# Optimization experiments

Hardware: AMD Instinct MI355X
Metric: run time of the kernel (lower is better)

Reference implementation:

```python
import jax, jax.numpy as jnp
import numpy as np

IMG_W, IMG_H = 960.0, 512.0
HM_W, HM_H = 240, 128
GRID_SIZE = (8000.0, 8000.0, 2000.0)
CUBE = (80, 80, 20)


def setup_inputs() -> dict:
    rng = np.random.default_rng(0)
    B, N, J = 8, 5, 15
    heatmaps = jnp.asarray(rng.random((B, N, J, HM_H, HM_W)).astype(np.float32))
    center3d = np.array([0.0, -500.0, 800.0])
    grid_center = jnp.asarray(np.tile(center3d.astype(np.float32), (B, 1)))
    Rs, Ts = [], []
    for v in range(N):  # cameras on a ring looking at the space center
        ang = 2.0 * np.pi * v / N
        cam_pos = center3d + np.array([5000.0 * np.cos(ang), 5000.0 * np.sin(ang), 1200.0])
        z = center3d - cam_pos; z = z / np.linalg.norm(z)
        x = np.cross(z, np.array([0.0, 0.0, 1.0])); x = x / np.linalg.norm(x)
        y = np.cross(z, x)
        Rs.append(np.stack([x, y, z])); Ts.append(cam_pos)
    R = jnp.asarray(np.tile(np.stack(Rs)[None], (B, 1, 1, 1)).astype(np.float32))
    T = jnp.asarray(np.tile(np.stack(Ts)[None], (B, 1, 1)).astype(np.float32))
    f = jnp.full((B, N, 2), 1500.0, jnp.float32)
    c = jnp.asarray(np.tile(np.array([IMG_W / 2, IMG_H / 2], np.float32), (B, N, 1)))
    k = jnp.asarray((1e-4 * rng.standard_normal((B, N, 3))).astype(np.float32))
    p = jnp.asarray((1e-4 * rng.standard_normal((B, N, 2))).astype(np.float32))
    cam_center = jnp.asarray(np.tile(np.array([IMG_W / 2, IMG_H / 2], np.float32), (B, N, 1)))
    scale = jnp.asarray(np.tile(np.array([IMG_W / 200.0, IMG_H / 200.0], np.float32), (B, N, 1)))
    return dict(heatmaps=heatmaps, grid_center=grid_center, R=R, T=T, f=f, c=c,
                k=k, p=p, cam_center=cam_center, scale=scale)


def _compute_grid(center):  # center [3] -> [nbins,3], meshgrid 'ij' like torch
    ax = [jnp.linspace(-GRID_SIZE[d] / 2, GRID_SIZE[d] / 2, CUBE[d]) + center[d] for d in range(3)]
    X, Y, Z = jnp.meshgrid(*ax, indexing='ij')
    return jnp.stack([X.ravel(), Y.ravel(), Z.ravel()], axis=1)


def _bilinear(img, x, y):  # img [J,H,W], x,y [N]; zero padding, align_corners=True
    x0 = jnp.floor(x); y0 = jnp.floor(y)
    dx = x - x0; dy = y - y0
    def tap(ix, iy, w):
        valid = (ix >= 0) & (ix < HM_W) & (iy >= 0) & (iy < HM_H)
        ii = jnp.clip(ix, 0, HM_W - 1).astype(jnp.int32)
        jj = jnp.clip(iy, 0, HM_H - 1).astype(jnp.int32)
        return img[:, jj, ii] * (w * valid)[None, :]
    return (tap(x0, y0, (1 - dx) * (1 - dy)) + tap(x0 + 1, y0, dx * (1 - dy)) +
            tap(x0, y0 + 1, (1 - dx) * dy) + tap(x0 + 1, y0 + 1, dx * dy))


def _per_cam(hm, grid, R, T, f, c, k, p, cc, sc):
    # pinhole projection with radial/tangential distortion (voxelpose project_pose)
    xcam = R @ (grid - T).T                       # [3,N]
    yn = xcam[:2] / (xcam[2] + 1e-5)              # [2,N]
    r2 = yn[0] ** 2 + yn[1] ** 2
    radial = 1.0 + k[0] * r2 + k[1] * r2 ** 2 + k[2] * r2 ** 3
    tan = p[0] * yn[1] + p[1] * yn[0]
    yd = yn * (radial + 2.0 * tan) + jnp.stack([p[1], p[0]])[:, None] * r2
    xy = (f[:, None] * yd + c[:, None]).T         # [N,2] pixel coords
    width = 2.0 * cc[0]; height = 2.0 * cc[1]
    mask = (xy[:, 0] >= 0) & (xy[:, 1] >= 0) & (xy[:, 0] < width) & (xy[:, 1] < height)
    xy = jnp.clip(xy, -1.0, jnp.maximum(width, height))
    # get_transform with rot=0: h = 200*scale[0]
    h200 = 200.0 * sc[0]
    res = jnp.array([IMG_W, IMG_H], jnp.float32)
    xy = xy * (res / h200) + res * (-cc / h200 + 0.5)
    xy = xy * jnp.array([HM_W, HM_H], jnp.float32) / res
    g = xy / jnp.array([HM_W - 1, HM_H - 1], jnp.float32) * 2.0 - 1.0
    g = jnp.clip(g, -1.1, 1.1)
    px = (g[:, 0] + 1.0) * 0.5 * (HM_W - 1)
    py = (g[:, 1] + 1.0) * 0.5 * (HM_H - 1)
    return _bilinear(hm, px, py), mask.astype(hm.dtype)  # [J,N], [N]


def _forward(heatmaps, grid_center, R, T, f, c, k, p, cam_center, scale):
    B, N, J = heatmaps.shape[:3]
    grids = jax.vmap(_compute_grid)(grid_center)  # [B,nbins,3]
    per_b = jax.vmap(_per_cam, in_axes=(0, None, 0, 0, 0, 0, 0, 0, 0, 0))
    vals, mask = jax.vmap(per_b)(heatmaps, grids, R, T, f, c, k, p, cam_center, scale)
    # vals [B,n,J,nbins], mask [B,n,nbins]: masked mean over cameras
    num = jnp.einsum('bnjv,bnv->bjv', vals, mask)
    den = jnp.sum(mask, axis=1) + 1e-6            # [B,nbins]
    cubes = num / den[:, None, :]
    cubes = jnp.nan_to_num(cubes)
    cubes = jnp.clip(cubes, 0.0, 1.0).reshape(B, J, *CUBE)
    return cubes, grids


def reference(heatmaps, grid_center, R, T, f, c, k, p, cam_center, scale):
    return _forward(heatmaps, grid_center, R, T, f, c, k, p, cam_center, scale)
```

## Files before the change

kernel.cpp:

```cpp
#include <hip/hip_runtime.h>

#define HM_W 240
#define HM_H 128
#define NCAM 5
#define NJ   15
#define CX   80
#define CY   80
#define CZ   20
#define NBINS (CX*CY*CZ)
#define NB   8
#define HWPIX (HM_H*HM_W)

__device__ __forceinline__ int iclamp(int x, int lo, int hi) {
    return x < lo ? lo : (x > hi ? hi : x);
}

#define PACK_CHUNKS ((NCAM * HWPIX) / 256)
__global__ void __launch_bounds__(256)
pack_u8(const float* __restrict__ hm, uint4* __restrict__ out)
{
    const int b = blockIdx.x & 7;
    const int chunk = blockIdx.x >> 3;
    const int pix = chunk * 256 + threadIdx.x;
    const int n = pix / HWPIX;
    const int yx = pix - n * HWPIX;
    const int bn = b * NCAM + n;
    const float* src = hm + (size_t)bn * NJ * HWPIX + yx;
    unsigned v8[16];
    #pragma unroll
    for (int j = 0; j < NJ; ++j) {
        float v = src[(size_t)j * HWPIX];
        v = fminf(fmaxf(v, 0.0f), 1.0f);
        v8[j] = (unsigned)fmaf(v, 255.0f, 0.5f);
    }
    v8[15] = 0u;
    uint4 q;
    q.x = v8[0]  | (v8[1]  << 8) | (v8[2]  << 16) | (v8[3]  << 24);
    q.y = v8[4]  | (v8[5]  << 8) | (v8[6]  << 16) | (v8[7]  << 24);
    q.z = v8[8]  | (v8[9]  << 8) | (v8[10] << 16) | (v8[11] << 24);
    q.w = v8[12] | (v8[13] << 8) | (v8[14] << 16);
    out[(size_t)bn * HWPIX + yx] = q;
}

struct TapsW {
    int i00, i10, i01, i11;
    unsigned W;
    float m;
};

__device__ __forceinline__ TapsW make_taps(
    float xc, float yc, float zc,
    float k0, float k1, float k2, float p0, float p1,
    float fx, float fy, float cxx, float cyy,
    float width, float height, float himax,
    float Ax, float Bx, float Ay, float By)
{
    const float inv = 1.0f / (zc + 1e-5f);
    const float yn0 = xc * inv;
    const float yn1 = yc * inv;
    const float r2 = yn0 * yn0 + yn1 * yn1;
    const float radial = 1.0f + k0 * r2 + k1 * (r2 * r2) + k2 * (r2 * r2 * r2);
    const float tan2 = 2.0f * (p0 * yn1 + p1 * yn0);
    const float yd0 = yn0 * (radial + tan2) + p1 * r2;
    const float yd1 = yn1 * (radial + tan2) + p0 * r2;

    float x = fmaf(fx, yd0, cxx);
    float y = fmaf(fy, yd1, cyy);

    const float m = (x >= 0.0f && y >= 0.0f && x < width && y < height) ? 1.0f : 0.0f;

    x = fminf(fmaxf(x, -1.0f), himax);
    y = fminf(fmaxf(y, -1.0f), himax);

    float gx = fmaf(Ax, x, Bx);
    float gy = fmaf(Ay, y, By);
    gx = fminf(fmaxf(gx, -1.1f), 1.1f);
    gy = fminf(fmaxf(gy, -1.1f), 1.1f);
    const float px = (gx + 1.0f) * (0.5f * (HM_W - 1));
    const float py = (gy + 1.0f) * (0.5f * (HM_H - 1));

    const float x0f = floorf(px), y0f = floorf(py);
    const float dx = px - x0f, dy = py - y0f;
    const int x0 = (int)x0f, y0 = (int)y0f;
    const int x1 = x0 + 1, y1 = y0 + 1;

    float w00 = (1.0f - dx) * (1.0f - dy);
    float w10 = dx * (1.0f - dy);
    float w01 = (1.0f - dx) * dy;
    float w11 = dx * dy;

    const bool vx0 = (x0 >= 0) & (x0 < HM_W);
    const bool vx1 = (x1 >= 0) & (x1 < HM_W);
    const bool vy0 = (y0 >= 0) & (y0 < HM_H);
    const bool vy1 = (y1 >= 0) & (y1 < HM_H);

    w00 = (vx0 && vy0) ? w00 * m : 0.0f;
    w10 = (vx1 && vy0) ? w10 * m : 0.0f;
    w01 = (vx0 && vy1) ? w01 * m : 0.0f;
    w11 = (vx1 && vy1) ? w11 * m : 0.0f;

    const unsigned wq0 = (unsigned)fmaf(w00, 255.0f, 0.5f);
    const unsigned wq1 = (unsigned)fmaf(w10, 255.0f, 0.5f);
    const unsigned wq2 = (unsigned)fmaf(w01, 255.0f, 0.5f);
    const unsigned wq3 = (unsigned)fmaf(w11, 255.0f, 0.5f);

    TapsW t;
    t.W = wq0 | (wq1 << 8) | (wq2 << 16) | (wq3 << 24);
    t.m = m;

    const int xa = iclamp(x0, 0, HM_W - 1);
    const int xb = iclamp(x1, 0, HM_W - 1);
    const int ya = iclamp(y0, 0, HM_H - 1);
    const int yb = iclamp(y1, 0, HM_H - 1);

    t.i00 = ya * HM_W + xa;
    t.i10 = ya * HM_W + xb;
    t.i01 = yb * HM_W + xa;
    t.i11 = yb * HM_W + xb;
    return t;
}

struct CamLoad {
    uint4 a00, a10, a01, a11;
    uint4 b00, b10, b01, b11;
    unsigned W0, W1;
    float m0, m1;
};

__device__ __forceinline__ CamLoad issue_cam(
    const uint4* __restrict__ hmp, int bn,
    float gx, float gy, float gz0, float gz1,
    const float* __restrict__ R, const float* __restrict__ T,
    const float* __restrict__ f, const float* __restrict__ c,
    const float* __restrict__ k, const float* __restrict__ p,
    const float* __restrict__ cc, const float* __restrict__ sc)
{
    const float* Rn = R + (size_t)bn * 9;
    const float* Tn = T + (size_t)bn * 3;

    const float X = gx - Tn[0];
    const float Y = gy - Tn[1];
    const float Z0 = gz0 - Tn[2];
    const float Z1 = gz1 - Tn[2];

    const float xp = Rn[0] * X + Rn[1] * Y;
    const float yp = Rn[3] * X + Rn[4] * Y;
    const float zp = Rn[6] * X + Rn[7] * Y;

    const float k0 = k[bn * 3 + 0], k1 = k[bn * 3 + 1], k2 = k[bn * 3 + 2];
    const float p0 = p[bn * 2 + 0], p1 = p[bn * 2 + 1];
    const float fx = f[bn * 2 + 0], fy = f[bn * 2 + 1];
    const float cxx = c[bn * 2 + 0], cyy = c[bn * 2 + 1];
    const float ccx = cc[bn * 2 + 0], ccy = cc[bn * 2 + 1];
    const float width = 2.0f * ccx, height = 2.0f * ccy;
    const float himax = fmaxf(width, height);

    const float inv_h = 1.0f / (200.0f * sc[bn * 2 + 0]);
    const float Ax = (2.0f * (float)HM_W / (float)(HM_W - 1)) * inv_h;
    const float Bx = (0.5f - ccx * inv_h) * (2.0f * (float)HM_W / (float)(HM_W - 1)) - 1.0f;
    const float Ay = (2.0f * (float)HM_H / (float)(HM_H - 1)) * inv_h;
    const float By = (0.5f - ccy * inv_h) * (2.0f * (float)HM_H / (float)(HM_H - 1)) - 1.0f;

    const TapsW t0 = make_taps(fmaf(Rn[2], Z0, xp), fmaf(Rn[5], Z0, yp), fmaf(Rn[8], Z0, zp),
                               k0, k1, k2, p0, p1, fx, fy, cxx, cyy,
                               width, height, himax, Ax, Bx, Ay, By);
    const TapsW t1 = make_taps(fmaf(Rn[2], Z1, xp), fmaf(Rn[5], Z1, yp), fmaf(Rn[8], Z1, zp),
                               k0, k1, k2, p0, p1, fx, fy, cxx, cyy,
                               width, height, himax, Ax, Bx, Ay, By);

    const uint4* base = hmp + (size_t)bn * HWPIX;
    CamLoad L;
    L.a00 = base[t0.i00]; L.a10 = base[t0.i10];
    L.a01 = base[t0.i01]; L.a11 = base[t0.i11];
    L.b00 = base[t1.i00]; L.b10 = base[t1.i10];
    L.b01 = base[t1.i01]; L.b11 = base[t1.i11];
    L.W0 = t0.W; L.W1 = t1.W;
    L.m0 = t0.m; L.m1 = t1.m;
    return L;
}

__device__ __forceinline__ void dot_taps(uint4 q00, uint4 q10, uint4 q01, uint4 q11,
                                         unsigned W, unsigned* __restrict__ acc)
{
    const unsigned* a00 = (const unsigned*)&q00;
    const unsigned* a10 = (const unsigned*)&q10;
    const unsigned* a01 = (const unsigned*)&q01;
    const unsigned* a11 = (const unsigned*)&q11;
    #pragma unroll
    for (int d = 0; d < 4; ++d) {
        const int jb = 4 * d;
        const unsigned pA = __builtin_amdgcn_perm(a00[d], a10[d], 0x01050004u);
        const unsigned pB = __builtin_amdgcn_perm(a01[d], a11[d], 0x01050004u);
        acc[jb + 0] = __builtin_amdgcn_udot4(
            __builtin_amdgcn_perm(pA, pB, 0x01000504u), W, acc[jb + 0], false);
        acc[jb + 1] = __builtin_amdgcn_udot4(
            __builtin_amdgcn_perm(pA, pB, 0x03020706u), W, acc[jb + 1], false);
        const unsigned pC = __builtin_amdgcn_perm(a00[d], a10[d], 0x03070206u);
        const unsigned pD = __builtin_amdgcn_perm(a01[d], a11[d], 0x03070206u);
        acc[jb + 2] = __builtin_amdgcn_udot4(
            __builtin_amdgcn_perm(pC, pD, 0x01000504u), W, acc[jb + 2], false);
        if (jb + 3 < NJ)
            acc[jb + 3] = __builtin_amdgcn_udot4(
                __builtin_amdgcn_perm(pC, pD, 0x03020706u), W, acc[jb + 3], false);
    }
}

__device__ __forceinline__ void consume(const CamLoad& L,
                                        unsigned* __restrict__ acc0,
                                        unsigned* __restrict__ acc1,
                                        float& den0, float& den1)
{
    dot_taps(L.a00, L.a10, L.a01, L.a11, L.W0, acc0);
    dot_taps(L.b00, L.b10, L.b01, L.b11, L.W1, acc1);
    den0 += L.m0;
    den1 += L.m1;
}

#define PROJ_CHUNKS ((NBINS / 2) / 256)
__global__ void __launch_bounds__(256)
project_u8(const uint4* __restrict__ hmp,
           const float* __restrict__ grid_center,
           const float* __restrict__ R, const float* __restrict__ T,
           const float* __restrict__ f, const float* __restrict__ c,
           const float* __restrict__ k, const float* __restrict__ p,
           const float* __restrict__ cc, const float* __restrict__ sc,
           float* __restrict__ cubes, float* __restrict__ grids)
{
    const int b = blockIdx.x & 7;
    const int chunk = blockIdx.x >> 3;
    const int v2 = chunk * 256 + threadIdx.x;

    const int col = v2 / (CZ / 2);
    const int tz  = v2 - col * (CZ / 2);
    const int ix = col / CY;
    const int iy = col - ix * CY;
    const int iz0 = 2 * tz;
    const int v0 = col * CZ + iz0;

    const float gcx = grid_center[b * 3 + 0];
    const float gcy = grid_center[b * 3 + 1];
    const float gcz = grid_center[b * 3 + 2];

    const float gx = -4000.0f + (float)ix * (8000.0f / 79.0f) + gcx;
    const float gy = -4000.0f + (float)iy * (8000.0f / 79.0f) + gcy;
    const float gz0 = -1000.0f + (float)iz0 * (2000.0f / 19.0f) + gcz;
    const float gz1 = gz0 + (2000.0f / 19.0f);

    {
        float* g = grids + ((size_t)b * NBINS + v0) * 3;
        float2* g2 = reinterpret_cast<float2*>(g);
        g2[0] = make_float2(gx, gy);
        g2[1] = make_float2(gz0, gx);
        g2[2] = make_float2(gy, gz1);
    }

    unsigned acc0[NJ], acc1[NJ];
    #pragma unroll
    for (int j = 0; j < NJ; ++j) { acc0[j] = 0u; acc1[j] = 0u; }
    float den0 = 1e-6f, den1 = 1e-6f;

    const int bn0 = b * NCAM;

    CamLoad A = issue_cam(hmp, bn0 + 0, gx, gy, gz0, gz1, R, T, f, c, k, p, cc, sc);
    CamLoad Bv = issue_cam(hmp, bn0 + 1, gx, gy, gz0, gz1, R, T, f, c, k, p, cc, sc);

    consume(A, acc0, acc1, den0, den1);
    A = issue_cam(hmp, bn0 + 2, gx, gy, gz0, gz1, R, T, f, c, k, p, cc, sc);

    consume(Bv, acc0, acc1, den0, den1);
    Bv = issue_cam(hmp, bn0 + 3, gx, gy, gz0, gz1, R, T, f, c, k, p, cc, sc);

    consume(A, acc0, acc1, den0, den1);
    A = issue_cam(hmp, bn0 + 4, gx, gy, gz0, gz1, R, T, f, c, k, p, cc, sc);

    consume(Bv, acc0, acc1, den0, den1);
    consume(A, acc0, acc1, den0, den1);

    const float s0 = (1.0f / 65025.0f) / den0;
    const float s1 = (1.0f / 65025.0f) / den1;
    const size_t outbase = (size_t)b * NJ * NBINS + v0;
    #pragma unroll
    for (int j = 0; j < NJ; ++j) {
        float2 o;
        o.x = fminf((float)acc0[j] * s0, 1.0f);
        o.y = fminf((float)acc1[j] * s1, 1.0f);
        *reinterpret_cast<float2*>(cubes + outbase + (size_t)j * NBINS) = o;
    }
}

__global__ void __launch_bounds__(256)
project_direct(const float* __restrict__ hm,
               const float* __restrict__ grid_center,
               const float* __restrict__ R, const float* __restrict__ T,
               const float* __restrict__ f, const float* __restrict__ c,
               const float* __restrict__ k, const float* __restrict__ p,
               const float* __restrict__ cc, const float* __restrict__ sc,
               float* __restrict__ cubes, float* __restrict__ grids)
{
    const int b = blockIdx.y;
    const int v = blockIdx.x * blockDim.x + threadIdx.x;
    if (v >= NBINS) return;

    const int ix = v / (CY * CZ);
    const int rem = v - ix * (CY * CZ);
    const int iy = rem / CZ;
    const int iz = rem - iy * CZ;

    const float gx = -4000.0f + (float)ix * (8000.0f / 79.0f) + grid_center[b * 3 + 0];
    const float gy = -4000.0f + (float)iy * (8000.0f / 79.0f) + grid_center[b * 3 + 1];
    const float gz = -1000.0f + (float)iz * (2000.0f / 19.0f) + grid_center[b * 3 + 2];

    {
        float* g = grids + ((size_t)b * NBINS + v) * 3;
        g[0] = gx; g[1] = gy; g[2] = gz;
    }

    float num[NJ];
    #pragma unroll
    for (int j = 0; j < NJ; ++j) num[j] = 0.0f;
    float den = 1e-6f;

    for (int n = 0; n < NCAM; ++n) {
        const int bn = b * NCAM + n;
        const float* Rn = R + (size_t)bn * 9;
        const float* Tn = T + (size_t)bn * 3;
        const float X = gx - Tn[0], Y = gy - Tn[1], Z = gz - Tn[2];

        const float xc = Rn[0]*X + Rn[1]*Y + Rn[2]*Z;
        const float yc = Rn[3]*X + Rn[4]*Y + Rn[5]*Z;
        const float zc = Rn[6]*X + Rn[7]*Y + Rn[8]*Z;

        const float inv = 1.0f / (zc + 1e-5f);
        const float yn0 = xc * inv, yn1 = yc * inv;
        const float r2 = yn0*yn0 + yn1*yn1;
        const float k0 = k[bn*3+0], k1 = k[bn*3+1], k2 = k[bn*3+2];
        const float radial = 1.0f + k0*r2 + k1*r2*r2 + k2*r2*r2*r2;
        const float p0 = p[bn*2+0], p1 = p[bn*2+1];
        const float tan2 = 2.0f * (p0*yn1 + p1*yn0);
        const float yd0 = yn0*(radial+tan2) + p1*r2;
        const float yd1 = yn1*(radial+tan2) + p0*r2;

        float x = fmaf(f[bn*2+0], yd0, c[bn*2+0]);
        float y = fmaf(f[bn*2+1], yd1, c[bn*2+1]);

        const float ccx = cc[bn*2+0], ccy = cc[bn*2+1];
        const float width = 2.0f*ccx, height = 2.0f*ccy;
        const float m = (x >= 0.0f && y >= 0.0f && x < width && y < height) ? 1.0f : 0.0f;
        const float himax = fmaxf(width, height);
        x = fminf(fmaxf(x, -1.0f), himax);
        y = fminf(fmaxf(y, -1.0f), himax);

        const float inv_h = 1.0f / (200.0f * sc[bn*2+0]);
        float gxn = (x*inv_h + (0.5f - ccx*inv_h)) * (2.0f*(float)HM_W/(float)(HM_W-1)) - 1.0f;
        float gyn = (y*inv_h + (0.5f - ccy*inv_h)) * (2.0f*(float)HM_H/(float)(HM_H-1)) - 1.0f;
        gxn = fminf(fmaxf(gxn, -1.1f), 1.1f);
        gyn = fminf(fmaxf(gyn, -1.1f), 1.1f);
        const float px = (gxn + 1.0f) * (0.5f * (HM_W - 1));
        const float py = (gyn + 1.0f) * (0.5f * (HM_H - 1));

        const float x0f = floorf(px), y0f = floorf(py);
        const float dx = px - x0f, dy = py - y0f;
        const int x0 = (int)x0f, y0 = (int)y0f;
        const int x1 = x0 + 1, y1 = y0 + 1;

        float w00 = (1.0f-dx)*(1.0f-dy), w10 = dx*(1.0f-dy);
        float w01 = (1.0f-dx)*dy,        w11 = dx*dy;
        const bool vx0 = (x0 >= 0) & (x0 < HM_W);
        const bool vx1 = (x1 >= 0) & (x1 < HM_W);
        const bool vy0 = (y0 >= 0) & (y0 < HM_H);
        const bool vy1 = (y1 >= 0) & (y1 < HM_H);
        w00 = (vx0 && vy0) ? w00*m : 0.0f;
        w10 = (vx1 && vy0) ? w10*m : 0.0f;
        w01 = (vx0 && vy1) ? w01*m : 0.0f;
        w11 = (vx1 && vy1) ? w11*m : 0.0f;

        const int xa = iclamp(x0,0,HM_W-1), xb = iclamp(x1,0,HM_W-1);
        const int ya = iclamp(y0,0,HM_H-1), yb = iclamp(y1,0,HM_H-1);
        const int i00 = ya*HM_W+xa, i10 = ya*HM_W+xb, i01 = yb*HM_W+xa, i11 = yb*HM_W+xb;

        const float* base = hm + (size_t)bn * NJ * HWPIX;
        #pragma unroll
        for (int j = 0; j < NJ; ++j) {
            const float* img = base + (size_t)j * HWPIX;
            num[j] += w00*img[i00] + w10*img[i10] + w01*img[i01] + w11*img[i11];
        }
        den += m;
    }

    const float invden = 1.0f / den;
    const size_t outbase = (size_t)b * NJ * NBINS + v;
    #pragma unroll
    for (int j = 0; j < NJ; ++j) {
        float val = num[j] * invden;
        val = fminf(fmaxf(val, 0.0f), 1.0f);
        cubes[outbase + (size_t)j * NBINS] = val;
    }
}

extern "C" void kernel_launch(void* const* d_in, const int* in_sizes, int n_in,
                              void* d_out, int out_size, void* d_ws, size_t ws_size,
                              hipStream_t stream) {
    const float* hm = (const float*)d_in[0];
    const float* gc = (const float*)d_in[1];
    const float* R  = (const float*)d_in[2];
    const float* T  = (const float*)d_in[3];
    const float* f  = (const float*)d_in[4];
    const float* c  = (const float*)d_in[5];
    const float* k  = (const float*)d_in[6];
    const float* p  = (const float*)d_in[7];
    const float* cc = (const float*)d_in[8];
    const float* sc = (const float*)d_in[9];

    float* out   = (float*)d_out;
    float* cubes = out;
    float* grids = out + (size_t)NB * NJ * NBINS;

    const size_t need = (size_t)NB * NCAM * HWPIX * 16 + 64;
    if (ws_size >= need) {
        uint4* hmp = (uint4*)d_ws;
        hipLaunchKernelGGL(pack_u8, dim3(NB * PACK_CHUNKS), dim3(256), 0, stream,
                           hm, hmp);
        hipLaunchKernelGGL(project_u8, dim3(NB * PROJ_CHUNKS), dim3(256), 0, stream,
                           hmp, gc, R, T, f, c, k, p, cc, sc, cubes, grids);
    } else {
        dim3 grid((NBINS + 255) / 256, NB);
        hipLaunchKernelGGL(project_direct, grid, dim3(256), 0, stream,
                           hm, gc, R, T, f, c, k, p, cc, sc, cubes, grids);
    }
}
```

Measured before the change: 58.47 us.

## Pack vertically-paired heatmap texels so each bilinear column fetch is one 32-byte load

The pack kernel now writes each texel together with the texel one row below into a 32-byte pair. The projection kernel can then fetch both vertical taps of a bilinear sample as one contiguous 32-byte read per column, with a select for the top-row edge case. This halves the number of gather instructions, at the cost of doubling the packed workspace and its write traffic. Heatmap loads and output stores are also made nontemporal, the camera loop is simplified, and the older 16-byte path is kept as a fallback when the workspace is too small.

New measurement: 85.61 us. 1.46x slower.

```diff
diff --git a/kernel.cpp b/kernel.cpp
--- a/kernel.cpp
+++ b/kernel.cpp
@@ -1,4 +1,5 @@
 #include <hip/hip_runtime.h>
+#include <string.h>
 
 #define HM_W 240
 #define HM_H 128
@@ -15,21 +16,30 @@
     return x < lo ? lo : (x > hi ? hi : x);
 }
 
+__device__ __forceinline__ uint4 sel4(bool c, uint4 a, uint4 b) {
+    uint4 r;
+    r.x = c ? a.x : b.x;  r.y = c ? a.y : b.y;
+    r.z = c ? a.z : b.z;  r.w = c ? a.w : b.w;
+    return r;
+}
+
+
 #define PACK_CHUNKS ((NCAM * HWPIX) / 256)
 __global__ void __launch_bounds__(256)
-pack_u8(const float* __restrict__ hm, uint4* __restrict__ out)
+pack_vp(const float* __restrict__ hm, uint4* __restrict__ vp)
 {
     const int b = blockIdx.x & 7;
     const int chunk = blockIdx.x >> 3;
     const int pix = chunk * 256 + threadIdx.x;
     const int n = pix / HWPIX;
     const int yx = pix - n * HWPIX;
+    const int y = yx / HM_W;
     const int bn = b * NCAM + n;
     const float* src = hm + (size_t)bn * NJ * HWPIX + yx;
     unsigned v8[16];
     #pragma unroll
     for (int j = 0; j < NJ; ++j) {
-        float v = src[(size_t)j * HWPIX];
+        float v = __builtin_nontemporal_load(src + (size_t)j * HWPIX);
         v = fminf(fmaxf(v, 0.0f), 1.0f);
         v8[j] = (unsigned)fmaf(v, 255.0f, 0.5f);
     }
@@ -39,16 +49,21 @@
     q.y = v8[4]  | (v8[5]  << 8) | (v8[6]  << 16) | (v8[7]  << 24);
     q.z = v8[8]  | (v8[9]  << 8) | (v8[10] << 16) | (v8[11] << 24);
     q.w = v8[12] | (v8[13] << 8) | (v8[14] << 16);
-    out[(size_t)bn * HWPIX + yx] = q;
-}
-
-struct TapsW {
-    int i00, i10, i01, i11;
+
+    uint4* e = vp + ((size_t)bn * HWPIX + yx) * 2;
+    e[0] = q;
+    if (y > 0)      (e - 2 * HM_W)[1] = q;
+    if (y == HM_H - 1) e[1] = q;
+}
+
+struct TapsV {
+    int e0, e1;
     unsigned W;
     float m;
+    bool selB;
 };
 
-__device__ __forceinline__ TapsW make_taps(
+__device__ __forceinline__ TapsV make_tapsv(
     float xc, float yc, float zc,
     float k0, float k1, float k2, float p0, float p1,
     float fx, float fy, float cxx, float cyy,
@@ -104,79 +119,17 @@
     const unsigned wq2 = (unsigned)fmaf(w01, 255.0f, 0.5f);
     const unsigned wq3 = (unsigned)fmaf(w11, 255.0f, 0.5f);
 
-    TapsW t;
+    TapsV t;
     t.W = wq0 | (wq1 << 8) | (wq2 << 16) | (wq3 << 24);
     t.m = m;
+    t.selB = (y0 >= 0);
 
     const int xa = iclamp(x0, 0, HM_W - 1);
     const int xb = iclamp(x1, 0, HM_W - 1);
     const int ya = iclamp(y0, 0, HM_H - 1);
-    const int yb = iclamp(y1, 0, HM_H - 1);
-
-    t.i00 = ya * HM_W + xa;
-    t.i10 = ya * HM_W + xb;
-    t.i01 = yb * HM_W + xa;
-    t.i11 = yb * HM_W + xb;
+    t.e0 = ya * HM_W + xa;
+    t.e1 = ya * HM_W + xb;
     return t;
-}
-
-struct CamLoad {
-    uint4 a00, a10, a01, a11;
-    uint4 b00, b10, b01, b11;
-    unsigned W0, W1;
-    float m0, m1;
-};
-
-__device__ __forceinline__ CamLoad issue_cam(
-    const uint4* __restrict__ hmp, int bn,
-    float gx, float gy, float gz0, float gz1,
-    const float* __restrict__ R, const float* __restrict__ T,
-    const float* __restrict__ f, const float* __restrict__ c,
-    const float* __restrict__ k, const float* __restrict__ p,
-    const float* __restrict__ cc, const float* __restrict__ sc)
-{
-    const float* Rn = R + (size_t)bn * 9;
-    const float* Tn = T + (size_t)bn * 3;
-
-    const float X = gx - Tn[0];
-    const float Y = gy - Tn[1];
-    const float Z0 = gz0 - Tn[2];
-    const float Z1 = gz1 - Tn[2];
-
-    const float xp = Rn[0] * X + Rn[1] * Y;
-    const float yp = Rn[3] * X + Rn[4] * Y;
-    const float zp = Rn[6] * X + Rn[7] * Y;
-
-    const float k0 = k[bn * 3 + 0], k1 = k[bn * 3 + 1], k2 = k[bn * 3 + 2];
-    const float p0 = p[bn * 2 + 0], p1 = p[bn * 2 + 1];
-    const float fx = f[bn * 2 + 0], fy = f[bn * 2 + 1];
-    const float cxx = c[bn * 2 + 0], cyy = c[bn * 2 + 1];
-    const float ccx = cc[bn * 2 + 0], ccy = cc[bn * 2 + 1];
-    const float width = 2.0f * ccx, height = 2.0f * ccy;
-    const float himax = fmaxf(width, height);
-
-    const float inv_h = 1.0f / (200.0f * sc[bn * 2 + 0]);
-    const float Ax = (2.0f * (float)HM_W / (float)(HM_W - 1)) * inv_h;
-    const float Bx = (0.5f - ccx * inv_h) * (2.0f * (float)HM_W / (float)(HM_W - 1)) - 1.0f;
-    const float Ay = (2.0f * (float)HM_H / (float)(HM_H - 1)) * inv_h;
-    const float By = (0.5f - ccy * inv_h) * (2.0f * (float)HM_H / (float)(HM_H - 1)) - 1.0f;
-
-    const TapsW t0 = make_taps(fmaf(Rn[2], Z0, xp), fmaf(Rn[5], Z0, yp), fmaf(Rn[8], Z0, zp),
-                               k0, k1, k2, p0, p1, fx, fy, cxx, cyy,
-                               width, height, himax, Ax, Bx, Ay, By);
-    const TapsW t1 = make_taps(fmaf(Rn[2], Z1, xp), fmaf(Rn[5], Z1, yp), fmaf(Rn[8], Z1, zp),
-                               k0, k1, k2, p0, p1, fx, fy, cxx, cyy,
-                               width, height, himax, Ax, Bx, Ay, By);
-
-    const uint4* base = hmp + (size_t)bn * HWPIX;
-    CamLoad L;
-    L.a00 = base[t0.i00]; L.a10 = base[t0.i10];
-    L.a01 = base[t0.i01]; L.a11 = base[t0.i11];
-    L.b00 = base[t1.i00]; L.b10 = base[t1.i10];
-    L.b01 = base[t1.i01]; L.b11 = base[t1.i11];
-    L.W0 = t0.W; L.W1 = t1.W;
-    L.m0 = t0.m; L.m1 = t1.m;
-    return L;
 }
 
 __device__ __forceinline__ void dot_taps(uint4 q00, uint4 q10, uint4 q01, uint4 q11,
@@ -205,18 +158,216 @@
     }
 }
 
-__device__ __forceinline__ void consume(const CamLoad& L,
-                                        unsigned* __restrict__ acc0,
-                                        unsigned* __restrict__ acc1,
-                                        float& den0, float& den1)
-{
-    dot_taps(L.a00, L.a10, L.a01, L.a11, L.W0, acc0);
-    dot_taps(L.b00, L.b10, L.b01, L.b11, L.W1, acc1);
-    den0 += L.m0;
-    den1 += L.m1;
-}
-
 #define PROJ_CHUNKS ((NBINS / 2) / 256)
+__global__ void __launch_bounds__(256)
+project_vp(const uint4* __restrict__ vp,
+           const float* __restrict__ grid_center,
+           const float* __restrict__ R, const float* __restrict__ T,
+           const float* __restrict__ f, const float* __restrict__ c,
+           const float* __restrict__ k, const float* __restrict__ p,
+           const float* __restrict__ cc, const float* __restrict__ sc,
+           float* __restrict__ cubes, float* __restrict__ grids)
+{
+    const int b = blockIdx.x & 7;
+    const int chunk = blockIdx.x >> 3;
+    const int v2 = chunk * 256 + threadIdx.x;
+
+    const int col = v2 / (CZ / 2);
+    const int tz  = v2 - col * (CZ / 2);
+    const int ix = col / CY;
+    const int iy = col - ix * CY;
+    const int iz0 = 2 * tz;
+    const int v0 = col * CZ + iz0;
+
+    const float gcx = grid_center[b * 3 + 0];
+    const float gcy = grid_center[b * 3 + 1];
+    const float gcz = grid_center[b * 3 + 2];
+
+    const float gx = -4000.0f + (float)ix * (8000.0f / 79.0f) + gcx;
+    const float gy = -4000.0f + (float)iy * (8000.0f / 79.0f) + gcy;
+    const float gz0 = -1000.0f + (float)iz0 * (2000.0f / 19.0f) + gcz;
+    const float gz1 = gz0 + (2000.0f / 19.0f);
+
+    {
+        float* g = grids + ((size_t)b * NBINS + v0) * 3;
+        union { float2 f2; double d; } u0, u1, u2;
+        u0.f2 = make_float2(gx, gy);
+        u1.f2 = make_float2(gz0, gx);
+        u2.f2 = make_float2(gy, gz1);
+        __builtin_nontemporal_store(u0.d, (double*)(g + 0));
+        __builtin_nontemporal_store(u1.d, (double*)(g + 2));
+        __builtin_nontemporal_store(u2.d, (double*)(g + 4));
+    }
+
+    unsigned acc0[NJ], acc1[NJ];
+    #pragma unroll
+    for (int j = 0; j < NJ; ++j) { acc0[j] = 0u; acc1[j] = 0u; }
+    float den0 = 1e-6f, den1 = 1e-6f;
+
+    #pragma unroll
+    for (int n = 0; n < NCAM; ++n) {
+        const int bn = b * NCAM + n;
+        const float* Rn = R + (size_t)bn * 9;
+        const float* Tn = T + (size_t)bn * 3;
+
+        const float X = gx - Tn[0];
+        const float Y = gy - Tn[1];
+        const float Z0 = gz0 - Tn[2];
+        const float Z1 = gz1 - Tn[2];
+
+        const float xp = Rn[0] * X + Rn[1] * Y;
+        const float yp = Rn[3] * X + Rn[4] * Y;
+        const float zp = Rn[6] * X + Rn[7] * Y;
+
+        const float k0 = k[bn * 3 + 0], k1 = k[bn * 3 + 1], k2 = k[bn * 3 + 2];
+        const float p0 = p[bn * 2 + 0], p1 = p[bn * 2 + 1];
+        const float fx = f[bn * 2 + 0], fy = f[bn * 2 + 1];
+        const float cxx = c[bn * 2 + 0], cyy = c[bn * 2 + 1];
+        const float ccx = cc[bn * 2 + 0], ccy = cc[bn * 2 + 1];
+        const float width = 2.0f * ccx, height = 2.0f * ccy;
+        const float himax = fmaxf(width, height);
+
+        const float inv_h = 1.0f / (200.0f * sc[bn * 2 + 0]);
+        const float Ax = (2.0f * (float)HM_W / (float)(HM_W - 1)) * inv_h;
+        const float Bx = (0.5f - ccx * inv_h) * (2.0f * (float)HM_W / (float)(HM_W - 1)) - 1.0f;
+        const float Ay = (2.0f * (float)HM_H / (float)(HM_H - 1)) * inv_h;
+        const float By = (0.5f - ccy * inv_h) * (2.0f * (float)HM_H / (float)(HM_H - 1)) - 1.0f;
+
+        const TapsV t0 = make_tapsv(fmaf(Rn[2], Z0, xp), fmaf(Rn[5], Z0, yp), fmaf(Rn[8], Z0, zp),
+                                    k0, k1, k2, p0, p1, fx, fy, cxx, cyy,
+                                    width, height, himax, Ax, Bx, Ay, By);
+        const TapsV t1 = make_tapsv(fmaf(Rn[2], Z1, xp), fmaf(Rn[5], Z1, yp), fmaf(Rn[8], Z1, zp),
+                                    k0, k1, k2, p0, p1, fx, fy, cxx, cyy,
+                                    width, height, himax, Ax, Bx, Ay, By);
+
+        const uint4* base = vp + (size_t)bn * HWPIX * 2;
+
+        const uint4* e00 = base + 2 * t0.e0;
+        const uint4* e01 = base + 2 * t0.e1;
+        const uint4 a0lo = e00[0], a0hi = e00[1];
+        const uint4 a1lo = e01[0], a1hi = e01[1];
+        const uint4* e10 = base + 2 * t1.e0;
+        const uint4* e11 = base + 2 * t1.e1;
+        const uint4 b0lo = e10[0], b0hi = e10[1];
+        const uint4 b1lo = e11[0], b1hi = e11[1];
+
+        const uint4 qa0b = sel4(t0.selB, a0hi, a0lo);
+        const uint4 qa1b = sel4(t0.selB, a1hi, a1lo);
+        const uint4 qb0b = sel4(t1.selB, b0hi, b0lo);
+        const uint4 qb1b = sel4(t1.selB, b1hi, b1lo);
+
+        dot_taps(a0lo, a1lo, qa0b, qa1b, t0.W, acc0);
+        dot_taps(b0lo, b1lo, qb0b, qb1b, t1.W, acc1);
+        den0 += t0.m;
+        den1 += t1.m;
+    }
+
+    const float s0 = (1.0f / 65025.0f) / den0;
+    const float s1 = (1.0f / 65025.0f) / den1;
+    const size_t outbase = (size_t)b * NJ * NBINS + v0;
+    #pragma unroll
+    for (int j = 0; j < NJ; ++j) {
+        union { float2 f2; double d; } o;
+        o.f2.x = fminf((float)acc0[j] * s0, 1.0f);
+        o.f2.y = fminf((float)acc1[j] * s1, 1.0f);
+        __builtin_nontemporal_store(o.d, (double*)(cubes + outbase + (size_t)j * NBINS));
+    }
+}
+
+
+__global__ void __launch_bounds__(256)
+pack_u8(const float* __restrict__ hm, uint4* __restrict__ out)
+{
+    const int b = blockIdx.x & 7;
+    const int chunk = blockIdx.x >> 3;
+    const int pix = chunk * 256 + threadIdx.x;
+    const int n = pix / HWPIX;
+    const int yx = pix - n * HWPIX;
+    const int bn = b * NCAM + n;
+    const float* src = hm + (size_t)bn * NJ * HWPIX + yx;
+    unsigned v8[16];
+    #pragma unroll
+    for (int j = 0; j < NJ; ++j) {
+        float v = src[(size_t)j * HWPIX];
+        v = fminf(fmaxf(v, 0.0f), 1.0f);
+        v8[j] = (unsigned)fmaf(v, 255.0f, 0.5f);
+    }
+    v8[15] = 0u;
+    uint4 q;
+    q.x = v8[0]  | (v8[1]  << 8) | (v8[2]  << 16) | (v8[3]  << 24);
+    q.y = v8[4]  | (v8[5]  << 8) | (v8[6]  << 16) | (v8[7]  << 24);
+    q.z = v8[8]  | (v8[9]  << 8) | (v8[10] << 16) | (v8[11] << 24);
+    q.w = v8[12] | (v8[13] << 8) | (v8[14] << 16);
+    out[(size_t)bn * HWPIX + yx] = q;
+}
+
+struct TapsU {
+    int i00, i10, i01, i11;
+    unsigned W;
+    float m;
+};
+
+__device__ __forceinline__ TapsU make_taps16(
+    float xc, float yc, float zc,
+    float k0, float k1, float k2, float p0, float p1,
+    float fx, float fy, float cxx, float cyy,
+    float width, float height, float himax,
+    float Ax, float Bx, float Ay, float By)
+{
+    const float inv = 1.0f / (zc + 1e-5f);
+    const float yn0 = xc * inv;
+    const float yn1 = yc * inv;
+    const float r2 = yn0 * yn0 + yn1 * yn1;
+    const float radial = 1.0f + k0 * r2 + k1 * (r2 * r2) + k2 * (r2 * r2 * r2);
+    const float tan2 = 2.0f * (p0 * yn1 + p1 * yn0);
+    const float yd0 = yn0 * (radial + tan2) + p1 * r2;
+    const float yd1 = yn1 * (radial + tan2) + p0 * r2;
+
+    float x = fmaf(fx, yd0, cxx);
+    float y = fmaf(fy, yd1, cyy);
+    const float m = (x >= 0.0f && y >= 0.0f && x < width && y < height) ? 1.0f : 0.0f;
+    x = fminf(fmaxf(x, -1.0f), himax);
+    y = fminf(fmaxf(y, -1.0f), himax);
+    float gx = fmaf(Ax, x, Bx);
+    float gy = fmaf(Ay, y, By);
+    gx = fminf(fmaxf(gx, -1.1f), 1.1f);
+    gy = fminf(fmaxf(gy, -1.1f), 1.1f);
+    const float px = (gx + 1.0f) * (0.5f * (HM_W - 1));
+    const float py = (gy + 1.0f) * (0.5f * (HM_H - 1));
+    const float x0f = floorf(px), y0f = floorf(py);
+    const float dx = px - x0f, dy = py - y0f;
+    const int x0 = (int)x0f, y0 = (int)y0f;
+    const int x1 = x0 + 1, y1 = y0 + 1;
+    float w00 = (1.0f - dx) * (1.0f - dy);
+    float w10 = dx * (1.0f - dy);
+    float w01 = (1.0f - dx) * dy;
+    float w11 = dx * dy;
+    const bool vx0 = (x0 >= 0) & (x0 < HM_W);
+    const bool vx1 = (x1 >= 0) & (x1 < HM_W);
+    const bool vy0 = (y0 >= 0) & (y0 < HM_H);
+    const bool vy1 = (y1 >= 0) & (y1 < HM_H);
+    w00 = (vx0 && vy0) ? w00 * m : 0.0f;
+    w10 = (vx1 && vy0) ? w10 * m : 0.0f;
+    w01 = (vx0 && vy1) ? w01 * m : 0.0f;
+    w11 = (vx1 && vy1) ? w11 * m : 0.0f;
+    const unsigned wq0 = (unsigned)fmaf(w00, 255.0f, 0.5f);
+    const unsigned wq1 = (unsigned)fmaf(w10, 255.0f, 0.5f);
+    const unsigned wq2 = (unsigned)fmaf(w01, 255.0f, 0.5f);
+    const unsigned wq3 = (unsigned)fmaf(w11, 255.0f, 0.5f);
+    TapsU t;
+    t.W = wq0 | (wq1 << 8) | (wq2 << 16) | (wq3 << 24);
+    t.m = m;
+    const int xa = iclamp(x0, 0, HM_W - 1);
+    const int xb = iclamp(x1, 0, HM_W - 1);
+    const int ya = iclamp(y0, 0, HM_H - 1);
+    const int yb = iclamp(y1, 0, HM_H - 1);
+    t.i00 = ya * HM_W + xa;
+    t.i10 = ya * HM_W + xb;
+    t.i01 = yb * HM_W + xa;
+    t.i11 = yb * HM_W + xb;
+    return t;
+}
+
 __global__ void __launch_bounds__(256)
 project_u8(const uint4* __restrict__ hmp,
            const float* __restrict__ grid_center,
@@ -259,22 +410,43 @@
     for (int j = 0; j < NJ; ++j) { acc0[j] = 0u; acc1[j] = 0u; }
     float den0 = 1e-6f, den1 = 1e-6f;
 
-    const int bn0 = b * NCAM;
-
-    CamLoad A = issue_cam(hmp, bn0 + 0, gx, gy, gz0, gz1, R, T, f, c, k, p, cc, sc);
-    CamLoad Bv = issue_cam(hmp, bn0 + 1, gx, gy, gz0, gz1, R, T, f, c, k, p, cc, sc);
-
-    consume(A, acc0, acc1, den0, den1);
-    A = issue_cam(hmp, bn0 + 2, gx, gy, gz0, gz1, R, T, f, c, k, p, cc, sc);
-
-    consume(Bv, acc0, acc1, den0, den1);
-    Bv = issue_cam(hmp, bn0 + 3, gx, gy, gz0, gz1, R, T, f, c, k, p, cc, sc);
-
-    consume(A, acc0, acc1, den0, den1);
-    A = issue_cam(hmp, bn0 + 4, gx, gy, gz0, gz1, R, T, f, c, k, p, cc, sc);
-
-    consume(Bv, acc0, acc1, den0, den1);
-    consume(A, acc0, acc1, den0, den1);
+    for (int n = 0; n < NCAM; ++n) {
+        const int bn = b * NCAM + n;
+        const float* Rn = R + (size_t)bn * 9;
+        const float* Tn = T + (size_t)bn * 3;
+        const float X = gx - Tn[0];
+        const float Y = gy - Tn[1];
+        const float Z0 = gz0 - Tn[2];
+        const float Z1 = gz1 - Tn[2];
+        const float xp = Rn[0] * X + Rn[1] * Y;
+        const float yp = Rn[3] * X + Rn[4] * Y;
+        const float zp = Rn[6] * X + Rn[7] * Y;
+        const float k0 = k[bn * 3 + 0], k1 = k[bn * 3 + 1], k2 = k[bn * 3 + 2];
+        const float p0 = p[bn * 2 + 0], p1 = p[bn * 2 + 1];
+        const float fx = f[bn * 2 + 0], fy = f[bn * 2 + 1];
+        const float cxx = c[bn * 2 + 0], cyy = c[bn * 2 + 1];
+        const float ccx = cc[bn * 2 + 0], ccy = cc[bn * 2 + 1];
+        const float width = 2.0f * ccx, height = 2.0f * ccy;
+        const float himax = fmaxf(width, height);
+        const float inv_h = 1.0f / (200.0f * sc[bn * 2 + 0]);
+        const float Ax = (2.0f * (float)HM_W / (float)(HM_W - 1)) * inv_h;
+        const float Bx = (0.5f - ccx * inv_h) * (2.0f * (float)HM_W / (float)(HM_W - 1)) - 1.0f;
+        const float Ay = (2.0f * (float)HM_H / (float)(HM_H - 1)) * inv_h;
+        const float By = (0.5f - ccy * inv_h) * (2.0f * (float)HM_H / (float)(HM_H - 1)) - 1.0f;
+
+        const TapsU t0 = make_taps16(fmaf(Rn[2], Z0, xp), fmaf(Rn[5], Z0, yp), fmaf(Rn[8], Z0, zp),
+                                     k0, k1, k2, p0, p1, fx, fy, cxx, cyy,
+                                     width, height, himax, Ax, Bx, Ay, By);
+        const TapsU t1 = make_taps16(fmaf(Rn[2], Z1, xp), fmaf(Rn[5], Z1, yp), fmaf(Rn[8], Z1, zp),
+                                     k0, k1, k2, p0, p1, fx, fy, cxx, cyy,
+                                     width, height, himax, Ax, Bx, Ay, By);
+
+        const uint4* base = hmp + (size_t)bn * HWPIX;
+        dot_taps(base[t0.i00], base[t0.i10], base[t0.i01], base[t0.i11], t0.W, acc0);
+        dot_taps(base[t1.i00], base[t1.i10], base[t1.i01], base[t1.i11], t1.W, acc1);
+        den0 += t0.m;
+        den1 += t1.m;
+    }
 
     const float s0 = (1.0f / 65025.0f) / den0;
     const float s1 = (1.0f / 65025.0f) / den1;
@@ -415,8 +587,15 @@
     float* cubes = out;
     float* grids = out + (size_t)NB * NJ * NBINS;
 
-    const size_t need = (size_t)NB * NCAM * HWPIX * 16 + 64;
-    if (ws_size >= need) {
+    const size_t need_vp = (size_t)NB * NCAM * HWPIX * 32 + 64;
+    const size_t need_16 = (size_t)NB * NCAM * HWPIX * 16 + 64;
+    if (ws_size >= need_vp) {
+        uint4* vp = (uint4*)d_ws;
+        hipLaunchKernelGGL(pack_vp, dim3(NB * PACK_CHUNKS), dim3(256), 0, stream,
+                           hm, vp);
+        hipLaunchKernelGGL(project_vp, dim3(NB * PROJ_CHUNKS), dim3(256), 0, stream,
+                           vp, gc, R, T, f, c, k, p, cc, sc, cubes, grids);
+    } else if (ws_size >= need_16) {
         uint4* hmp = (uint4*)d_ws;
         hipLaunchKernelGGL(pack_u8, dim3(NB * PACK_CHUNKS), dim3(256), 0, stream,
                            hm, hmp);
```
